# Kernel optimization log

Measured on AMD Instinct MI355X. Metric: run time of the kernel, lower is better.

Reference implementation:

```python
import jax, jax.numpy as jnp
import numpy as np

N = 12        # ALL_QUBITS
COM_Q = 9     # COM_QUBITS
IMG_Q = 11    # IMG_QUBITS
LAYERS = 2
SQRT2 = float(np.sqrt(2.0))
H_GATE = jnp.asarray([[1.0, 1.0], [1.0, -1.0]], dtype=jnp.complex64) / SQRT2


def _bitrev_perm(q):
    # column j of the wires-1..q subspace corresponds to param index bitrev(j)
    idx = np.arange(2 ** q)
    rev = np.zeros_like(idx)
    for bpos in range(q):
        rev |= ((idx >> bpos) & 1) << (q - 1 - bpos)
    return rev


def _apply_1q(state, U, w):
    # state: (B, 2^N) complex; apply 2x2 gate U on wire w (wire 0 = MSB)
    B = state.shape[0]
    s = state.reshape(B, 2 ** w, 2, -1)
    return jnp.einsum('ij,bpjq->bpiq', U, s).reshape(B, -1)


def _apply_cnot(state, c, t):
    B = state.shape[0]
    s = state.reshape((B,) + (2,) * N)
    s0 = jax.lax.slice_in_dim(s, 0, 1, axis=c + 1)
    s1 = jnp.flip(jax.lax.slice_in_dim(s, 1, 2, axis=c + 1), axis=t + 1)
    return jnp.concatenate([s0, s1], axis=c + 1).reshape(B, -1)


def _frqi(state, angles, q):
    # Hadamards on wires 1..q, then uniformly-controlled RY(angles) on wire 0
    for w in range(1, q + 1):
        state = _apply_1q(state, H_GATE, w)
    rev = _bitrev_perm(q)
    half = 0.5 * angles[:, rev]            # (B, 2^q), angle per control column
    c = jnp.cos(half)[:, :, None]
    s = jnp.sin(half)[:, :, None]
    B = state.shape[0]
    st = state.reshape(B, 2, 2 ** q, -1)   # (B, wire0, wires1..q, rest)
    new0 = c * st[:, 0] - s * st[:, 1]
    new1 = s * st[:, 0] + c * st[:, 1]
    return jnp.stack([new0, new1], axis=1).reshape(B, -1)


def _rot(phi, theta, omega):
    # PennyLane Rot = RZ(omega) RY(theta) RZ(phi)
    c = jnp.cos(theta / 2)
    s = jnp.sin(theta / 2)
    m00 = jnp.exp(-0.5j * (phi + omega)) * c
    m01 = -jnp.exp(0.5j * (phi - omega)) * s
    m10 = jnp.exp(-0.5j * (phi - omega)) * s
    m11 = jnp.exp(0.5j * (phi + omega)) * c
    return jnp.stack([jnp.stack([m00, m01]), jnp.stack([m10, m11])])


def _circuit(com_params, img_params, qp):
    B = com_params.shape[0]
    state = jnp.zeros((B, 2 ** N), jnp.complex64).at[:, 0].set(1.0)
    state = _frqi(state, com_params, COM_Q)
    for l in range(LAYERS):  # StronglyEntanglingLayers
        for w in range(N):
            state = _apply_1q(state, _rot(qp[l, w, 0], qp[l, w, 1], qp[l, w, 2]), w)
        r = l % (N - 1) + 1  # default ranges
        for w in range(N):
            state = _apply_cnot(state, w, (w + r) % N)
    state = _frqi(state, img_params, IMG_Q)
    p = (jnp.abs(state.reshape(B, 2, -1)) ** 2).sum(axis=2)  # (B, 2) wire-0 probs
    return p[:, 1] - p[:, 0]  # expval of Hamiltonian = -1 * Z(0)


def setup_inputs() -> dict:
    key = jax.random.key(0)
    k1, k2, k3 = jax.random.split(key, 3)
    B = 1024
    x = jax.random.uniform(k1, (B, 2, 32, 32), dtype=jnp.float32)
    W = jax.random.normal(k2, (512, 2048), dtype=jnp.float32) * 0.02
    b = jnp.zeros((512,), dtype=jnp.float32)
    quantum_params = jax.random.uniform(k3, (LAYERS, N, 3), dtype=jnp.float32) * float(np.pi)
    return {"x": x, "W": W, "b": b, "quantum_params": quantum_params}


def reference(x, W, b, quantum_params):
    B = x.shape[0]
    xf = x.reshape(B, -1)                 # (B, 2048) img_params
    com = xf @ W.T + b                    # (B, 512) classical_nn output
    return _circuit(com, xf, quantum_params)
```

## Files before the change

kernel.cpp:

```cpp
#include <hip/hip_runtime.h>
#include <hip/hip_bf16.h>
#include <math.h>

#define RS2f 0.70710678118654752f

typedef __attribute__((ext_vector_type(8))) short bf16x8;
typedef __attribute__((ext_vector_type(4))) float f32x4;

__device__ __forceinline__ float bf2f(unsigned short h) {
    return __uint_as_float(((unsigned)h) << 16);
}
__device__ __forceinline__ ushort2 pk2(float a, float b) {
    union { __hip_bfloat162 h; ushort2 s; } u;
    u.h = __float22bfloat162_rn(make_float2(a, b));
    return u.s;
}

struct CMat { float m00r,m00i,m01r,m01i,m10r,m10i,m11r,m11i; };

__device__ __forceinline__ CMat mk_rot(const float* __restrict__ qp, int l, int w) {
    const float* g = qp + (l * 12 + w) * 3;
    float phi = g[0], th = g[1], om = g[2];
    float st, ct, sa, ca, sb, cb;
    sincosf(0.5f * th, &st, &ct);
    sincosf(0.5f * (phi + om), &sa, &ca);
    sincosf(0.5f * (phi - om), &sb, &cb);
    CMat M;
    M.m00r =  ct * ca; M.m00i = -ct * sa;
    M.m01r = -st * cb; M.m01i = -st * sb;
    M.m10r =  st * cb; M.m10i = -st * sb;
    M.m11r =  ct * ca; M.m11i =  ct * sa;
    return M;
}

__global__ __launch_bounds__(512) void gemm_fused(const float* __restrict__ A,
                                                  const float* __restrict__ B,
                                                  float* __restrict__ P,
                                                  const float* __restrict__ qp,
                                                  CMat* __restrict__ cmg) {
    __shared__ short As[128 * 136];
    __shared__ short Bs[128 * 136];
    const int tid = threadIdx.x, lane = tid & 63, wv = tid >> 6;
    const int quad = lane >> 4, mrow = lane & 15;
    const int bid = blockIdx.x;
    if (bid == 0 && tid < 24) cmg[tid] = mk_rot(qp, tid / 12, tid % 12);
    const int zt  = bid & 7;
    const int idx = bid >> 3;
    const int mt  = idx & 7, nt = idx >> 3;
    const int m0 = mt * 128, n0 = nt * 128;
    const int kb = zt * 256;
    const int srow = tid >> 2;
    const int sc = (tid & 3) * 16;

    f32x4 acc[8];
    #pragma unroll
    for (int j = 0; j < 8; ++j) acc[j] = (f32x4){0.f, 0.f, 0.f, 0.f};

    const float* Arow = A + (size_t)(m0 + srow) * 2048 + kb + sc;
    const float* Brow = B + (size_t)(n0 + srow) * 2048 + kb + sc;

    float4 av[4], bv[4];
    #pragma unroll
    for (int i = 0; i < 4; ++i) { av[i] = *(const float4*)(Arow + 4*i);
                                  bv[i] = *(const float4*)(Brow + 4*i); }

    for (int ch = 0; ch < 4; ++ch) {
        __syncthreads();
        #pragma unroll
        for (int i = 0; i < 4; ++i) {
            ushort2 h0 = pk2(av[i].x, av[i].y);
            ushort2 h1 = pk2(av[i].z, av[i].w);
            ushort2 l0 = pk2(av[i].x - bf2f(h0.x), av[i].y - bf2f(h0.y));
            ushort2 l1 = pk2(av[i].z - bf2f(h1.x), av[i].w - bf2f(h1.y));
            *(ushort4*)&As[srow * 136 + sc + 4*i]      = make_ushort4(h0.x, h0.y, h1.x, h1.y);
            *(ushort4*)&As[srow * 136 + 64 + sc + 4*i] = make_ushort4(l0.x, l0.y, l1.x, l1.y);
            h0 = pk2(bv[i].x, bv[i].y);
            h1 = pk2(bv[i].z, bv[i].w);
            l0 = pk2(bv[i].x - bf2f(h0.x), bv[i].y - bf2f(h0.y));
            l1 = pk2(bv[i].z - bf2f(h1.x), bv[i].w - bf2f(h1.y));
            *(ushort4*)&Bs[srow * 136 + sc + 4*i]      = make_ushort4(h0.x, h0.y, h1.x, h1.y);
            *(ushort4*)&Bs[srow * 136 + 64 + sc + 4*i] = make_ushort4(l0.x, l0.y, l1.x, l1.y);
        }
        __syncthreads();
        if (ch + 1 < 4) {
            const int o = (ch + 1) * 64;
            #pragma unroll
            for (int i = 0; i < 4; ++i) { av[i] = *(const float4*)(Arow + o + 4*i);
                                          bv[i] = *(const float4*)(Brow + o + 4*i); }
        }
        #pragma unroll
        for (int s = 0; s < 4; ++s) {
            const int off = s * 32 + quad * 8;
            bf16x8 af = *(const bf16x8*)&As[(wv * 16 + mrow) * 136 + off];
            #pragma unroll
            for (int j = 0; j < 8; ++j) {
                bf16x8 bf = *(const bf16x8*)&Bs[(j * 16 + mrow) * 136 + off];
                acc[j] = __builtin_amdgcn_mfma_f32_16x16x32_bf16(af, bf, acc[j], 0, 0, 0);
            }
        }
    }
    float* Pz = P + (size_t)zt * 524288;
    #pragma unroll
    for (int j = 0; j < 8; ++j)
        #pragma unroll
        for (int r = 0; r < 4; ++r)
            Pz[(m0 + wv * 16 + quad * 4 + r) * 512 + n0 + j * 16 + mrow] = acc[j][r];
}

__global__ __launch_bounds__(256) void gemm_f32(const float* __restrict__ A,
                                                const float* __restrict__ W,
                                                float* __restrict__ C,
                                                const float* __restrict__ qp,
                                                CMat* __restrict__ cmg) {
    __shared__ float Asf[64][33];
    __shared__ float Bsf[32][33];
    const int tid = threadIdx.x;
    if (blockIdx.x == 0 && blockIdx.y == 0 && tid < 24)
        cmg[tid] = mk_rot(qp, tid / 12, tid % 12);
    const int m0 = blockIdx.x * 64;
    const int n0 = blockIdx.y * 32;
    const int tm = tid >> 4, tn = tid & 15;
    float acc[4][2] = {};
    for (int k0 = 0; k0 < 2048; k0 += 32) {
        #pragma unroll
        for (int i = 0; i < 8; ++i) {
            int idx = tid + i * 256;
            Asf[idx >> 5][idx & 31] = A[(m0 + (idx >> 5)) * 2048 + k0 + (idx & 31)];
        }
        #pragma unroll
        for (int i = 0; i < 4; ++i) {
            int idx = tid + i * 256;
            Bsf[idx >> 5][idx & 31] = W[(n0 + (idx >> 5)) * 2048 + k0 + (idx & 31)];
        }
        __syncthreads();
        #pragma unroll
        for (int kk = 0; kk < 32; ++kk) {
            float a0 = Asf[tm*4+0][kk], a1 = Asf[tm*4+1][kk];
            float a2 = Asf[tm*4+2][kk], a3 = Asf[tm*4+3][kk];
            float b0 = Bsf[tn*2+0][kk], b1 = Bsf[tn*2+1][kk];
            acc[0][0] += a0*b0; acc[0][1] += a0*b1;
            acc[1][0] += a1*b0; acc[1][1] += a1*b1;
            acc[2][0] += a2*b0; acc[2][1] += a2*b1;
            acc[3][0] += a3*b0; acc[3][1] += a3*b1;
        }
        __syncthreads();
    }
    #pragma unroll
    for (int r = 0; r < 4; ++r)
        #pragma unroll
        for (int c = 0; c < 2; ++c)
            C[(m0 + tm*4 + r) * 512 + n0 + tn*2 + c] = acc[r][c];
}

template<int W> struct WI {
    static constexpr int kind = (W == 0 || W == 7) ? 2 : ((W >= 1 && W <= 6) ? 1 : 0);
    static constexpr int eb   = (W >= 8) ? (11 - W) : 0;
    static constexpr int lm   = (W >= 1 && W <= 6) ? (1 << (6 - W)) : 0;
    static constexpr int vm   = (W == 0) ? 2 : ((W == 7) ? 1 : 0);
};

__device__ __forceinline__ void exch_put(float* xbuf, int slot,
                                         const float vr[16], const float vi[16]) {
    __syncthreads();
    float4* p = (float4*)xbuf;
    #pragma unroll
    for (int j = 0; j < 8; ++j)
        p[(j << 8) + slot] = make_float4(vr[2*j], vi[2*j], vr[2*j+1], vi[2*j+1]);
    __syncthreads();
}

__device__ __forceinline__ void shfl_perm(float vr[16], float vi[16], int src) {
    #pragma unroll
    for (int e = 0; e < 16; ++e) {
        vr[e] = __shfl(vr[e], src, 64);
        vi[e] = __shfl(vi[e], src, 64);
    }
}

template<int EB>
__device__ __forceinline__ void rot_local(float vr[16], float vi[16], const CMat& M) {
    #pragma unroll
    for (int e = 0; e < 16; ++e) if (!(e & (1 << EB))) {
        const int e1 = e | (1 << EB);
        float x0r = vr[e],  x0i = vi[e];
        float x1r = vr[e1], x1i = vi[e1];
        vr[e]  = M.m00r*x0r - M.m00i*x0i + M.m01r*x1r - M.m01i*x1i;
        vi[e]  = M.m00r*x0i + M.m00i*x0r + M.m01r*x1i + M.m01i*x1r;
        vr[e1] = M.m10r*x0r - M.m10i*x0i + M.m11r*x1r - M.m11i*x1i;
        vi[e1] = M.m10r*x0i + M.m10i*x0r + M.m11r*x1i + M.m11i*x1r;
    }
}

template<int LM>
__device__ __forceinline__ void rot_lane(float vr[16], float vi[16], int lane, const CMat& M) {
    const bool hi = lane & LM;
    const float Ar = hi ? M.m11r : M.m00r, Ai = hi ? M.m11i : M.m00i;
    const float Br = hi ? M.m10r : M.m01r, Bi = hi ? M.m10i : M.m01i;
    #pragma unroll
    for (int e = 0; e < 16; ++e) {
        float pr = __shfl_xor(vr[e], LM, 64);
        float pi = __shfl_xor(vi[e], LM, 64);
        float orr = vr[e], oi = vi[e];
        vr[e] = Ar*orr - Ai*oi + Br*pr - Bi*pi;
        vi[e] = Ar*oi + Ai*orr + Br*pi + Bi*pr;
    }
}

template<int VM>
__device__ __forceinline__ void rot_wave(float vr[16], float vi[16], float* xbuf,
                                         int waveId, int lane, const CMat& M) {
    exch_put(xbuf, (waveId << 6) + lane, vr, vi);
    const float4* p = (const float4*)xbuf;
    const int ps = ((waveId ^ VM) << 6) + lane;
    const bool hi = waveId & VM;
    const float Ar = hi ? M.m11r : M.m00r, Ai = hi ? M.m11i : M.m00i;
    const float Br = hi ? M.m10r : M.m01r, Bi = hi ? M.m10i : M.m01i;
    #pragma unroll
    for (int j = 0; j < 8; ++j) {
        float4 q = p[(j << 8) + ps];
        const int e0 = 2*j, e1 = 2*j + 1;
        float r0 = vr[e0], i0 = vi[e0], r1 = vr[e1], i1 = vi[e1];
        vr[e0] = Ar*r0 - Ai*i0 + Br*q.x - Bi*q.y;
        vi[e0] = Ar*i0 + Ai*r0 + Br*q.y + Bi*q.x;
        vr[e1] = Ar*r1 - Ai*i1 + Br*q.z - Bi*q.w;
        vi[e1] = Ar*i1 + Ai*r1 + Br*q.w + Bi*q.z;
    }
}

template<int W>
__device__ __forceinline__ void rot_wire(float vr[16], float vi[16], float* xbuf,
                                         int waveId, int lane, const CMat& M) {
    if constexpr (WI<W>::kind == 0)      rot_local<WI<W>::eb>(vr, vi, M);
    else if constexpr (WI<W>::kind == 1) rot_lane<WI<W>::lm>(vr, vi, lane, M);
    else                                 rot_wave<WI<W>::vm>(vr, vi, xbuf, waveId, lane, M);
}

template<int C, int T>
__device__ __forceinline__ void cnot(float vr[16], float vi[16], float* xbuf,
                                     int waveId, int lane) {
    constexpr int ck = WI<C>::kind, tk = WI<T>::kind;
    if constexpr (ck == 0 && tk == 0) {
        constexpr int cb = 1 << WI<C>::eb, tb = 1 << WI<T>::eb;
        #pragma unroll
        for (int e = 0; e < 16; ++e) if ((e & cb) && !(e & tb)) {
            const int e1 = e | tb;
            float t = vr[e]; vr[e] = vr[e1]; vr[e1] = t;
            t = vi[e]; vi[e] = vi[e1]; vi[e1] = t;
        }
    } else if constexpr (ck == 0 && tk == 1) {
        constexpr int cb = 1 << WI<C>::eb, tm = WI<T>::lm;
        #pragma unroll
        for (int e = 0; e < 16; ++e) if (e & cb) {
            vr[e] = __shfl_xor(vr[e], tm, 64);
            vi[e] = __shfl_xor(vi[e], tm, 64);
        }
    } else if constexpr (ck == 0 && tk == 2) {
        constexpr int cb = 1 << WI<C>::eb, vm = WI<T>::vm;
        exch_put(xbuf, (waveId << 6) + lane, vr, vi);
        const float4* p = (const float4*)xbuf;
        const int ps = ((waveId ^ vm) << 6) + lane;
        #pragma unroll
        for (int j = 0; j < 8; ++j) {
            if ((((2*j) & cb) != 0) || (((2*j+1) & cb) != 0)) {
                float4 q = p[(j << 8) + ps];
                if (((2*j) & cb) != 0)   { vr[2*j]   = q.x; vi[2*j]   = q.y; }
                if (((2*j+1) & cb) != 0) { vr[2*j+1] = q.z; vi[2*j+1] = q.w; }
            }
        }
    } else if constexpr (ck == 1 && tk == 0) {
        constexpr int cm = WI<C>::lm, tb = 1 << WI<T>::eb;
        const bool cc = lane & cm;
        #pragma unroll
        for (int e = 0; e < 16; ++e) if (!(e & tb)) {
            const int e1 = e | tb;
            float a = vr[e], bb = vr[e1];
            vr[e] = cc ? bb : a; vr[e1] = cc ? a : bb;
            a = vi[e]; bb = vi[e1];
            vi[e] = cc ? bb : a; vi[e1] = cc ? a : bb;
        }
    } else if constexpr (ck == 1 && tk == 1) {
        constexpr int cm = WI<C>::lm, tm = WI<T>::lm;
        const int src = (lane & cm) ? (lane ^ tm) : lane;
        shfl_perm(vr, vi, src);
    } else if constexpr (ck == 1 && tk == 2) {
        constexpr int cm = WI<C>::lm, vm = WI<T>::vm;
        exch_put(xbuf, (waveId << 6) + lane, vr, vi);
        const float4* p = (const float4*)xbuf;
        const int ps = ((waveId ^ vm) << 6) + lane;
        const bool take = lane & cm;
        #pragma unroll
        for (int j = 0; j < 8; ++j) {
            float4 q = p[(j << 8) + ps];
            vr[2*j]   = take ? q.x : vr[2*j];   vi[2*j]   = take ? q.y : vi[2*j];
            vr[2*j+1] = take ? q.z : vr[2*j+1]; vi[2*j+1] = take ? q.w : vi[2*j+1];
        }
    } else if constexpr (ck == 2 && tk == 0) {
        constexpr int vm = WI<C>::vm, tb = 1 << WI<T>::eb;
        if (waveId & vm) {
            #pragma unroll
            for (int e = 0; e < 16; ++e) if (!(e & tb)) {
                const int e1 = e | tb;
                float t = vr[e]; vr[e] = vr[e1]; vr[e1] = t;
                t = vi[e]; vi[e] = vi[e1]; vi[e1] = t;
            }
        }
    } else {
        constexpr int vm = WI<C>::vm, tm = WI<T>::lm;
        if (waveId & vm) {
            #pragma unroll
            for (int e = 0; e < 16; ++e) {
                vr[e] = __shfl_xor(vr[e], tm, 64);
                vi[e] = __shfl_xor(vi[e], tm, 64);
            }
        }
    }
}

template<int W>
__device__ __forceinline__ void h_wire(float vr[16], float vi[16], float* xbuf,
                                       int waveId, int lane) {
    if constexpr (WI<W>::kind == 0) {
        constexpr int tb = 1 << WI<W>::eb;
        #pragma unroll
        for (int e = 0; e < 16; ++e) if (!(e & tb)) {
            const int e1 = e | tb;
            float x0 = vr[e], x1 = vr[e1];
            vr[e] = (x0 + x1) * RS2f; vr[e1] = (x0 - x1) * RS2f;
            x0 = vi[e]; x1 = vi[e1];
            vi[e] = (x0 + x1) * RS2f; vi[e1] = (x0 - x1) * RS2f;
        }
    } else if constexpr (WI<W>::kind == 1) {
        constexpr int m = WI<W>::lm;
        const float sgn = (lane & m) ? -RS2f : RS2f;
        #pragma unroll
        for (int e = 0; e < 16; ++e) {
            float pr = __shfl_xor(vr[e], m, 64);
            float pi = __shfl_xor(vi[e], m, 64);
            vr[e] = pr * RS2f + vr[e] * sgn;
            vi[e] = pi * RS2f + vi[e] * sgn;
        }
    } else {
        constexpr int vm = WI<W>::vm;
        exch_put(xbuf, (waveId << 6) + lane, vr, vi);
        const float4* p = (const float4*)xbuf;
        const int ps = ((waveId ^ vm) << 6) + lane;
        const float sgn = (waveId & vm) ? -RS2f : RS2f;
        #pragma unroll
        for (int j = 0; j < 8; ++j) {
            float4 q = p[(j << 8) + ps];
            vr[2*j]   = q.x * RS2f + vr[2*j]   * sgn;
            vi[2*j]   = q.y * RS2f + vi[2*j]   * sgn;
            vr[2*j+1] = q.z * RS2f + vr[2*j+1] * sgn;
            vi[2*j+1] = q.w * RS2f + vi[2*j+1] * sgn;
        }
    }
}

__global__ __launch_bounds__(256) void circuit_red(const float* __restrict__ P,
                                                   const float* __restrict__ xf,
                                                   const CMat* __restrict__ cmg,
                                                   const float* __restrict__ bias,
                                                   float* __restrict__ out, int SK) {
    __shared__ float xbuf[8192];
    const int tid = threadIdx.x, lane = tid & 63, waveId = tid >> 6;
    const int b = blockIdx.x;
    {
        float2 s = ((const float2*)bias)[tid];
        for (int z = 0; z < SK; ++z) {
            float2 q = ((const float2*)(P + (size_t)z * 524288 + (size_t)b * 512))[tid];
            s.x += q.x; s.y += q.y;
        }
        ((float2*)xbuf)[tid] = s;
    }
    __syncthreads();
    float vr[16], vi[16];
    #pragma unroll
    for (int e = 0; e < 16; ++e) { vr[e] = 0.0f; vi[e] = 0.0f; }
    const float K9 = 0.044194173824159216f;
    #pragma unroll
    for (int m = 0; m < 4; ++m) {
        int j = (lane << 3) | ((waveId & 1) << 2) | m;
        int rj = (int)(__brev((unsigned)j) >> 23);
        float h = 0.5f * xbuf[rj];
        float s = __sinf(h), c = __cosf(h);
        vr[m << 2] = K9 * ((waveId & 2) ? s : c);
    }
    #pragma unroll 1
    for (int l = 0; l < 2; ++l) {
        const CMat* cl = cmg + l * 12;
        { CMat M = cl[0];  rot_wire<0 >(vr, vi, xbuf, waveId, lane, M); }
        { CMat M = cl[1];  rot_wire<1 >(vr, vi, xbuf, waveId, lane, M); }
        { CMat M = cl[2];  rot_wire<2 >(vr, vi, xbuf, waveId, lane, M); }
        { CMat M = cl[3];  rot_wire<3 >(vr, vi, xbuf, waveId, lane, M); }
        { CMat M = cl[4];  rot_wire<4 >(vr, vi, xbuf, waveId, lane, M); }
        { CMat M = cl[5];  rot_wire<5 >(vr, vi, xbuf, waveId, lane, M); }
        { CMat M = cl[6];  rot_wire<6 >(vr, vi, xbuf, waveId, lane, M); }
        { CMat M = cl[7];  rot_wire<7 >(vr, vi, xbuf, waveId, lane, M); }
        { CMat M = cl[8];  rot_wire<8 >(vr, vi, xbuf, waveId, lane, M); }
        { CMat M = cl[9];  rot_wire<9 >(vr, vi, xbuf, waveId, lane, M); }
        { CMat M = cl[10]; rot_wire<10>(vr, vi, xbuf, waveId, lane, M); }
        { CMat M = cl[11]; rot_wire<11>(vr, vi, xbuf, waveId, lane, M); }
        if (l == 0) {
            int j = lane;
            j ^= (j & 2)  ? 1  : 0;
            j ^= (j & 4)  ? 2  : 0;
            j ^= (j & 8)  ? 4  : 0;
            j ^= (j & 16) ? 8  : 0;
            j ^= (j & 32) ? 16 : 0;
            j ^= (waveId & 2) ? 32 : 0;
            shfl_perm(vr, vi, j);
            cnot<6,7>(vr,vi,xbuf,waveId,lane);   cnot<7,8>(vr,vi,xbuf,waveId,lane);
            cnot<8,9>(vr,vi,xbuf,waveId,lane);   cnot<9,10>(vr,vi,xbuf,waveId,lane);
            cnot<10,11>(vr,vi,xbuf,waveId,lane); cnot<11,0>(vr,vi,xbuf,waveId,lane);
        } else {
            int j = lane;
            j ^= (j & 4)  ? 1  : 0;
            j ^= (j & 8)  ? 2  : 0;
            j ^= (j & 16) ? 4  : 0;
            j ^= (j & 32) ? 8  : 0;
            j ^= (waveId & 2) ? 16 : 0;
            shfl_perm(vr, vi, j);
            cnot<5,7>(vr,vi,xbuf,waveId,lane);   cnot<6,8>(vr,vi,xbuf,waveId,lane);
            cnot<7,9>(vr,vi,xbuf,waveId,lane);   cnot<8,10>(vr,vi,xbuf,waveId,lane);
            cnot<9,11>(vr,vi,xbuf,waveId,lane);  cnot<10,0>(vr,vi,xbuf,waveId,lane);
            cnot<11,1>(vr,vi,xbuf,waveId,lane);
        }
    }
    h_wire<1>(vr,vi,xbuf,waveId,lane);  h_wire<2>(vr,vi,xbuf,waveId,lane);
    h_wire<3>(vr,vi,xbuf,waveId,lane);  h_wire<4>(vr,vi,xbuf,waveId,lane);
    h_wire<5>(vr,vi,xbuf,waveId,lane);  h_wire<6>(vr,vi,xbuf,waveId,lane);
    h_wire<7>(vr,vi,xbuf,waveId,lane);  h_wire<8>(vr,vi,xbuf,waveId,lane);
    h_wire<9>(vr,vi,xbuf,waveId,lane);  h_wire<10>(vr,vi,xbuf,waveId,lane);
    h_wire<11>(vr,vi,xbuf,waveId,lane);
    exch_put(xbuf, (waveId << 6) + lane, vr, vi);
    {
        const float* xrow = xf + (size_t)b * 2048;
        const float4* p = (const float4*)xbuf;
        const int ps = ((waveId ^ 2) << 6) + lane;
        const bool hi = waveId & 2;
        float acc = 0.0f;
        #pragma unroll
        for (int j = 0; j < 8; ++j) {
            float4 q = p[(j << 8) + ps];
            #pragma unroll
            for (int h = 0; h < 2; ++h) {
                const int e = 2*j + h;
                const float prr = h ? q.z : q.x;
                const float pii = h ? q.w : q.y;
                int v = (lane << 5) | ((waveId & 1) << 4) | e;
                int rv = (int)(__brev((unsigned)v) >> 21);
                float ha = 0.5f * xrow[rv];
                float s = __sinf(ha), c = __cosf(ha);
                float nr = hi ? (s*prr + c*vr[e]) : (c*vr[e] - s*prr);
                float ni = hi ? (s*pii + c*vi[e]) : (c*vi[e] - s*pii);
                acc += nr*nr + ni*ni;
            }
        }
        if (!hi) acc = -acc;
        #pragma unroll
        for (int off = 32; off > 0; off >>= 1) acc += __shfl_down(acc, off, 64);
        __syncthreads();
        if (lane == 0) xbuf[waveId] = acc;
        __syncthreads();
        if (tid == 0) out[b] = xbuf[0] + xbuf[1] + xbuf[2] + xbuf[3];
    }
}

extern "C" void kernel_launch(void* const* d_in, const int* in_sizes, int n_in,
                              void* d_out, int out_size, void* d_ws, size_t ws_size,
                              hipStream_t stream) {
    const float* x    = (const float*)d_in[0];
    const float* W    = (const float*)d_in[1];
    const float* bias = (const float*)d_in[2];
    const float* qp   = (const float*)d_in[3];
    float* out = (float*)d_out;

    const size_t SLAB = 2097152;
    const size_t CMSZ = 1024;
    float* P = (float*)d_ws;

    if (ws_size >= 8 * SLAB + CMSZ) {
        CMat* cmg = (CMat*)((char*)d_ws + 8 * SLAB);
        gemm_fused<<<256, 512, 0, stream>>>(x, W, P, qp, cmg);
        circuit_red<<<1024, 256, 0, stream>>>(P, x, cmg, bias, out, 8);
    } else {
        CMat* cmg = (CMat*)((char*)d_ws + SLAB);
        dim3 g(16, 16);
        gemm_f32<<<g, 256, 0, stream>>>(x, W, P, qp, cmg);
        circuit_red<<<1024, 256, 0, stream>>>(P, x, cmg, bias, out, 1);
    }
}
```

Measured before the change: 139.9 us.

## Fuse split-K GEMM and circuit simulation into one cooperative kernel with grid sync

Replaces the two-kernel sequence (split-K bf16x3 GEMM, then per-sample circuit simulation) with one cooperative kernel of 1024 blocks. Each block first computes a 64x64 GEMM tile for one K-slice, using an XCD-aware tile mapping, then all blocks meet at a grid-wide barrier. After that each block runs the circuit body for one batch row, reusing the same shared-memory buffer. This is meant to remove the gap between kernel launches and the tail of the first kernel. In exchange it needs all 1024 blocks resident at once (4 per CU), which caps registers for the circuit code and adds the cost of a grid sync. If the cooperative launch fails, it falls back to the old two kernels.

```diff
diff --git a/kernel.cpp b/kernel.cpp
--- a/kernel.cpp
+++ b/kernel.cpp
@@ -1,6 +1,9 @@
 #include <hip/hip_runtime.h>
+#include <hip/hip_cooperative_groups.h>
 #include <hip/hip_bf16.h>
 #include <math.h>
+
+namespace cg = cooperative_groups;
 
 #define RS2f 0.70710678118654752f
 
@@ -33,125 +36,6 @@
     return M;
 }
 
-__global__ __launch_bounds__(512) void gemm_fused(const float* __restrict__ A,
-                                                  const float* __restrict__ B,
-                                                  float* __restrict__ P,
-                                                  const float* __restrict__ qp,
-                                                  CMat* __restrict__ cmg) {
-    __shared__ short As[128 * 136];
-    __shared__ short Bs[128 * 136];
-    const int tid = threadIdx.x, lane = tid & 63, wv = tid >> 6;
-    const int quad = lane >> 4, mrow = lane & 15;
-    const int bid = blockIdx.x;
-    if (bid == 0 && tid < 24) cmg[tid] = mk_rot(qp, tid / 12, tid % 12);
-    const int zt  = bid & 7;
-    const int idx = bid >> 3;
-    const int mt  = idx & 7, nt = idx >> 3;
-    const int m0 = mt * 128, n0 = nt * 128;
-    const int kb = zt * 256;
-    const int srow = tid >> 2;
-    const int sc = (tid & 3) * 16;
-
-    f32x4 acc[8];
-    #pragma unroll
-    for (int j = 0; j < 8; ++j) acc[j] = (f32x4){0.f, 0.f, 0.f, 0.f};
-
-    const float* Arow = A + (size_t)(m0 + srow) * 2048 + kb + sc;
-    const float* Brow = B + (size_t)(n0 + srow) * 2048 + kb + sc;
-
-    float4 av[4], bv[4];
-    #pragma unroll
-    for (int i = 0; i < 4; ++i) { av[i] = *(const float4*)(Arow + 4*i);
-                                  bv[i] = *(const float4*)(Brow + 4*i); }
-
-    for (int ch = 0; ch < 4; ++ch) {
-        __syncthreads();
-        #pragma unroll
-        for (int i = 0; i < 4; ++i) {
-            ushort2 h0 = pk2(av[i].x, av[i].y);
-            ushort2 h1 = pk2(av[i].z, av[i].w);
-            ushort2 l0 = pk2(av[i].x - bf2f(h0.x), av[i].y - bf2f(h0.y));
-            ushort2 l1 = pk2(av[i].z - bf2f(h1.x), av[i].w - bf2f(h1.y));
-            *(ushort4*)&As[srow * 136 + sc + 4*i]      = make_ushort4(h0.x, h0.y, h1.x, h1.y);
-            *(ushort4*)&As[srow * 136 + 64 + sc + 4*i] = make_ushort4(l0.x, l0.y, l1.x, l1.y);
-            h0 = pk2(bv[i].x, bv[i].y);
-            h1 = pk2(bv[i].z, bv[i].w);
-            l0 = pk2(bv[i].x - bf2f(h0.x), bv[i].y - bf2f(h0.y));
-            l1 = pk2(bv[i].z - bf2f(h1.x), bv[i].w - bf2f(h1.y));
-            *(ushort4*)&Bs[srow * 136 + sc + 4*i]      = make_ushort4(h0.x, h0.y, h1.x, h1.y);
-            *(ushort4*)&Bs[srow * 136 + 64 + sc + 4*i] = make_ushort4(l0.x, l0.y, l1.x, l1.y);
-        }
-        __syncthreads();
-        if (ch + 1 < 4) {
-            const int o = (ch + 1) * 64;
-            #pragma unroll
-            for (int i = 0; i < 4; ++i) { av[i] = *(const float4*)(Arow + o + 4*i);
-                                          bv[i] = *(const float4*)(Brow + o + 4*i); }
-        }
-        #pragma unroll
-        for (int s = 0; s < 4; ++s) {
-            const int off = s * 32 + quad * 8;
-            bf16x8 af = *(const bf16x8*)&As[(wv * 16 + mrow) * 136 + off];
-            #pragma unroll
-            for (int j = 0; j < 8; ++j) {
-                bf16x8 bf = *(const bf16x8*)&Bs[(j * 16 + mrow) * 136 + off];
-                acc[j] = __builtin_amdgcn_mfma_f32_16x16x32_bf16(af, bf, acc[j], 0, 0, 0);
-            }
-        }
-    }
-    float* Pz = P + (size_t)zt * 524288;
-    #pragma unroll
-    for (int j = 0; j < 8; ++j)
-        #pragma unroll
-        for (int r = 0; r < 4; ++r)
-            Pz[(m0 + wv * 16 + quad * 4 + r) * 512 + n0 + j * 16 + mrow] = acc[j][r];
-}
-
-__global__ __launch_bounds__(256) void gemm_f32(const float* __restrict__ A,
-                                                const float* __restrict__ W,
-                                                float* __restrict__ C,
-                                                const float* __restrict__ qp,
-                                                CMat* __restrict__ cmg) {
-    __shared__ float Asf[64][33];
-    __shared__ float Bsf[32][33];
-    const int tid = threadIdx.x;
-    if (blockIdx.x == 0 && blockIdx.y == 0 && tid < 24)
-        cmg[tid] = mk_rot(qp, tid / 12, tid % 12);
-    const int m0 = blockIdx.x * 64;
-    const int n0 = blockIdx.y * 32;
-    const int tm = tid >> 4, tn = tid & 15;
-    float acc[4][2] = {};
-    for (int k0 = 0; k0 < 2048; k0 += 32) {
-        #pragma unroll
-        for (int i = 0; i < 8; ++i) {
-            int idx = tid + i * 256;
-            Asf[idx >> 5][idx & 31] = A[(m0 + (idx >> 5)) * 2048 + k0 + (idx & 31)];
-        }
-        #pragma unroll
-        for (int i = 0; i < 4; ++i) {
-            int idx = tid + i * 256;
-            Bsf[idx >> 5][idx & 31] = W[(n0 + (idx >> 5)) * 2048 + k0 + (idx & 31)];
-        }
-        __syncthreads();
-        #pragma unroll
-        for (int kk = 0; kk < 32; ++kk) {
-            float a0 = Asf[tm*4+0][kk], a1 = Asf[tm*4+1][kk];
-            float a2 = Asf[tm*4+2][kk], a3 = Asf[tm*4+3][kk];
-            float b0 = Bsf[tn*2+0][kk], b1 = Bsf[tn*2+1][kk];
-            acc[0][0] += a0*b0; acc[0][1] += a0*b1;
-            acc[1][0] += a1*b0; acc[1][1] += a1*b1;
-            acc[2][0] += a2*b0; acc[2][1] += a2*b1;
-            acc[3][0] += a3*b0; acc[3][1] += a3*b1;
-        }
-        __syncthreads();
-    }
-    #pragma unroll
-    for (int r = 0; r < 4; ++r)
-        #pragma unroll
-        for (int c = 0; c < 2; ++c)
-            C[(m0 + tm*4 + r) * 512 + n0 + tn*2 + c] = acc[r][c];
-}
-
 template<int W> struct WI {
     static constexpr int kind = (W == 0 || W == 7) ? 2 : ((W >= 1 && W <= 6) ? 1 : 0);
     static constexpr int eb   = (W >= 8) ? (11 - W) : 0;
@@ -356,14 +240,13 @@
     }
 }
 
-__global__ __launch_bounds__(256) void circuit_red(const float* __restrict__ P,
-                                                   const float* __restrict__ xf,
-                                                   const CMat* __restrict__ cmg,
-                                                   const float* __restrict__ bias,
-                                                   float* __restrict__ out, int SK) {
-    __shared__ float xbuf[8192];
+__device__ __forceinline__ void circuit_body(float* xbuf, int b,
+                                             const float* __restrict__ P,
+                                             const float* __restrict__ xf,
+                                             const CMat* __restrict__ cmg,
+                                             const float* __restrict__ bias,
+                                             float* __restrict__ out, int SK) {
     const int tid = threadIdx.x, lane = tid & 63, waveId = tid >> 6;
-    const int b = blockIdx.x;
     {
         float2 s = ((const float2*)bias)[tid];
         for (int z = 0; z < SK; ++z) {
@@ -466,6 +349,220 @@
     }
 }
 
+__global__ __launch_bounds__(256, 4) void fused_all(const float* __restrict__ A,
+                                                    const float* __restrict__ B,
+                                                    const float* __restrict__ bias,
+                                                    const float* __restrict__ qp,
+                                                    float* __restrict__ P,
+                                                    CMat* __restrict__ cmg,
+                                                    float* __restrict__ out) {
+    __shared__ __align__(16) char lds[34816];
+    short* As   = (short*)lds;
+    short* Bs   = (short*)(lds + 17408);
+    float* xbuf = (float*)lds;
+    const int tid = threadIdx.x, lane = tid & 63, wv = tid >> 6;
+    const int quad = lane >> 4, mrow = lane & 15;
+    const int bid = blockIdx.x;
+
+    if (bid == 0 && tid < 24) cmg[tid] = mk_rot(qp, tid / 12, tid % 12);
+    {
+        const int xcd = bid & 7;
+        const int idx = bid >> 3;
+        const int mt  = ((xcd >> 1) << 2) | (idx & 3);
+        const int nt  = ((xcd & 1) << 2) | ((idx >> 2) & 3);
+        const int zt  = idx >> 4;
+        const int m0 = mt * 64, n0 = nt * 64;
+        const int kb = zt * 256;
+        const int srow = tid >> 2;
+        const int sc = (tid & 3) * 16;
+
+        f32x4 acc[4];
+        #pragma unroll
+        for (int j = 0; j < 4; ++j) acc[j] = (f32x4){0.f, 0.f, 0.f, 0.f};
+
+        const float* Arow = A + (size_t)(m0 + srow) * 2048 + kb + sc;
+        const float* Brow = B + (size_t)(n0 + srow) * 2048 + kb + sc;
+
+        float4 av[4], bv[4];
+        #pragma unroll
+        for (int i = 0; i < 4; ++i) { av[i] = *(const float4*)(Arow + 4*i);
+                                      bv[i] = *(const float4*)(Brow + 4*i); }
+
+        for (int ch = 0; ch < 4; ++ch) {
+            __syncthreads();
+            #pragma unroll
+            for (int i = 0; i < 4; ++i) {
+                ushort2 h0 = pk2(av[i].x, av[i].y);
+                ushort2 h1 = pk2(av[i].z, av[i].w);
+                ushort2 l0 = pk2(av[i].x - bf2f(h0.x), av[i].y - bf2f(h0.y));
+                ushort2 l1 = pk2(av[i].z - bf2f(h1.x), av[i].w - bf2f(h1.y));
+                *(ushort4*)&As[srow * 136 + sc + 4*i]      = make_ushort4(h0.x, h0.y, h1.x, h1.y);
+                *(ushort4*)&As[srow * 136 + 64 + sc + 4*i] = make_ushort4(l0.x, l0.y, l1.x, l1.y);
+                h0 = pk2(bv[i].x, bv[i].y);
+                h1 = pk2(bv[i].z, bv[i].w);
+                l0 = pk2(bv[i].x - bf2f(h0.x), bv[i].y - bf2f(h0.y));
+                l1 = pk2(bv[i].z - bf2f(h1.x), bv[i].w - bf2f(h1.y));
+                *(ushort4*)&Bs[srow * 136 + sc + 4*i]      = make_ushort4(h0.x, h0.y, h1.x, h1.y);
+                *(ushort4*)&Bs[srow * 136 + 64 + sc + 4*i] = make_ushort4(l0.x, l0.y, l1.x, l1.y);
+            }
+            __syncthreads();
+            if (ch + 1 < 4) {
+                const int o = (ch + 1) * 64;
+                #pragma unroll
+                for (int i = 0; i < 4; ++i) { av[i] = *(const float4*)(Arow + o + 4*i);
+                                              bv[i] = *(const float4*)(Brow + o + 4*i); }
+            }
+            #pragma unroll
+            for (int s = 0; s < 4; ++s) {
+                const int off = s * 32 + quad * 8;
+                bf16x8 af = *(const bf16x8*)&As[(wv * 16 + mrow) * 136 + off];
+                #pragma unroll
+                for (int j = 0; j < 4; ++j) {
+                    bf16x8 bf = *(const bf16x8*)&Bs[(j * 16 + mrow) * 136 + off];
+                    acc[j] = __builtin_amdgcn_mfma_f32_16x16x32_bf16(af, bf, acc[j], 0, 0, 0);
+                }
+            }
+        }
+        float* Pz = P + (size_t)zt * 524288;
+        #pragma unroll
+        for (int j = 0; j < 4; ++j)
+            #pragma unroll
+            for (int r = 0; r < 4; ++r)
+                Pz[(m0 + wv * 16 + quad * 4 + r) * 512 + n0 + j * 16 + mrow] = acc[j][r];
+    }
+    __threadfence();
+    cg::this_grid().sync();
+    circuit_body(xbuf, bid, P, A, cmg, bias, out, 8);
+}
+
+__global__ __launch_bounds__(512) void gemm_fused(const float* __restrict__ A,
+                                                  const float* __restrict__ B,
+                                                  float* __restrict__ P,
+                                                  const float* __restrict__ qp,
+                                                  CMat* __restrict__ cmg) {
+    __shared__ short As[128 * 136];
+    __shared__ short Bs[128 * 136];
+    const int tid = threadIdx.x, lane = tid & 63, wv = tid >> 6;
+    const int quad = lane >> 4, mrow = lane & 15;
+    const int bid = blockIdx.x;
+    if (bid == 0 && tid < 24) cmg[tid] = mk_rot(qp, tid / 12, tid % 12);
+    const int zt  = bid & 7;
+    const int idx = bid >> 3;
+    const int mt  = idx & 7, nt = idx >> 3;
+    const int m0 = mt * 128, n0 = nt * 128;
+    const int kb = zt * 256;
+    const int srow = tid >> 2;
+    const int sc = (tid & 3) * 16;
+
+    f32x4 acc[8];
+    #pragma unroll
+    for (int j = 0; j < 8; ++j) acc[j] = (f32x4){0.f, 0.f, 0.f, 0.f};
+
+    const float* Arow = A + (size_t)(m0 + srow) * 2048 + kb + sc;
+    const float* Brow = B + (size_t)(n0 + srow) * 2048 + kb + sc;
+
+    float4 av[4], bv[4];
+    #pragma unroll
+    for (int i = 0; i < 4; ++i) { av[i] = *(const float4*)(Arow + 4*i);
+                                  bv[i] = *(const float4*)(Brow + 4*i); }
+
+    for (int ch = 0; ch < 4; ++ch) {
+        __syncthreads();
+        #pragma unroll
+        for (int i = 0; i < 4; ++i) {
+            ushort2 h0 = pk2(av[i].x, av[i].y);
+            ushort2 h1 = pk2(av[i].z, av[i].w);
+            ushort2 l0 = pk2(av[i].x - bf2f(h0.x), av[i].y - bf2f(h0.y));
+            ushort2 l1 = pk2(av[i].z - bf2f(h1.x), av[i].w - bf2f(h1.y));
+            *(ushort4*)&As[srow * 136 + sc + 4*i]      = make_ushort4(h0.x, h0.y, h1.x, h1.y);
+            *(ushort4*)&As[srow * 136 + 64 + sc + 4*i] = make_ushort4(l0.x, l0.y, l1.x, l1.y);
+            h0 = pk2(bv[i].x, bv[i].y);
+            h1 = pk2(bv[i].z, bv[i].w);
+            l0 = pk2(bv[i].x - bf2f(h0.x), bv[i].y - bf2f(h0.y));
+            l1 = pk2(bv[i].z - bf2f(h1.x), bv[i].w - bf2f(h1.y));
+            *(ushort4*)&Bs[srow * 136 + sc + 4*i]      = make_ushort4(h0.x, h0.y, h1.x, h1.y);
+            *(ushort4*)&Bs[srow * 136 + 64 + sc + 4*i] = make_ushort4(l0.x, l0.y, l1.x, l1.y);
+        }
+        __syncthreads();
+        if (ch + 1 < 4) {
+            const int o = (ch + 1) * 64;
+            #pragma unroll
+            for (int i = 0; i < 4; ++i) { av[i] = *(const float4*)(Arow + o + 4*i);
+                                          bv[i] = *(const float4*)(Brow + o + 4*i); }
+        }
+        #pragma unroll
+        for (int s = 0; s < 4; ++s) {
+            const int off = s * 32 + quad * 8;
+            bf16x8 af = *(const bf16x8*)&As[(wv * 16 + mrow) * 136 + off];
+            #pragma unroll
+            for (int j = 0; j < 8; ++j) {
+                bf16x8 bf = *(const bf16x8*)&Bs[(j * 16 + mrow) * 136 + off];
+                acc[j] = __builtin_amdgcn_mfma_f32_16x16x32_bf16(af, bf, acc[j], 0, 0, 0);
+            }
+        }
+    }
+    float* Pz = P + (size_t)zt * 524288;
+    #pragma unroll
+    for (int j = 0; j < 8; ++j)
+        #pragma unroll
+        for (int r = 0; r < 4; ++r)
+            Pz[(m0 + wv * 16 + quad * 4 + r) * 512 + n0 + j * 16 + mrow] = acc[j][r];
+}
+
+__global__ __launch_bounds__(256) void circuit_red(const float* __restrict__ P,
+                                                   const float* __restrict__ xf,
+                                                   const CMat* __restrict__ cmg,
+                                                   const float* __restrict__ bias,
+                                                   float* __restrict__ out, int SK) {
+    __shared__ float xbuf[8192];
+    circuit_body(xbuf, blockIdx.x, P, xf, cmg, bias, out, SK);
+}
+
+__global__ __launch_bounds__(256) void gemm_f32(const float* __restrict__ A,
+                                                const float* __restrict__ W,
+                                                float* __restrict__ C,
+                                                const float* __restrict__ qp,
+                                                CMat* __restrict__ cmg) {
+    __shared__ float Asf[64][33];
+    __shared__ float Bsf[32][33];
+    const int tid = threadIdx.x;
+    if (blockIdx.x == 0 && blockIdx.y == 0 && tid < 24)
+        cmg[tid] = mk_rot(qp, tid / 12, tid % 12);
+    const int m0 = blockIdx.x * 64;
+    const int n0 = blockIdx.y * 32;
+    const int tm = tid >> 4, tn = tid & 15;
+    float acc[4][2] = {};
+    for (int k0 = 0; k0 < 2048; k0 += 32) {
+        #pragma unroll
+        for (int i = 0; i < 8; ++i) {
+            int idx = tid + i * 256;
+            Asf[idx >> 5][idx & 31] = A[(m0 + (idx >> 5)) * 2048 + k0 + (idx & 31)];
+        }
+        #pragma unroll
+        for (int i = 0; i < 4; ++i) {
+            int idx = tid + i * 256;
+            Bsf[idx >> 5][idx & 31] = W[(n0 + (idx >> 5)) * 2048 + k0 + (idx & 31)];
+        }
+        __syncthreads();
+        #pragma unroll
+        for (int kk = 0; kk < 32; ++kk) {
+            float a0 = Asf[tm*4+0][kk], a1 = Asf[tm*4+1][kk];
+            float a2 = Asf[tm*4+2][kk], a3 = Asf[tm*4+3][kk];
+            float b0 = Bsf[tn*2+0][kk], b1 = Bsf[tn*2+1][kk];
+            acc[0][0] += a0*b0; acc[0][1] += a0*b1;
+            acc[1][0] += a1*b0; acc[1][1] += a1*b1;
+            acc[2][0] += a2*b0; acc[2][1] += a2*b1;
+            acc[3][0] += a3*b0; acc[3][1] += a3*b1;
+        }
+        __syncthreads();
+    }
+    #pragma unroll
+    for (int r = 0; r < 4; ++r)
+        #pragma unroll
+        for (int c = 0; c < 2; ++c)
+            C[(m0 + tm*4 + r) * 512 + n0 + tn*2 + c] = acc[r][c];
+}
+
 extern "C" void kernel_launch(void* const* d_in, const int* in_sizes, int n_in,
                               void* d_out, int out_size, void* d_ws, size_t ws_size,
                               hipStream_t stream) {
@@ -481,8 +578,16 @@
 
     if (ws_size >= 8 * SLAB + CMSZ) {
         CMat* cmg = (CMat*)((char*)d_ws + 8 * SLAB);
-        gemm_fused<<<256, 512, 0, stream>>>(x, W, P, qp, cmg);
-        circuit_red<<<1024, 256, 0, stream>>>(P, x, cmg, bias, out, 8);
+        void* args[] = { (void*)&x, (void*)&W, (void*)&bias, (void*)&qp,
+                         (void*)&P, (void*)&cmg, (void*)&out };
+        hipError_t e = hipLaunchCooperativeKernel((const void*)fused_all,
+                                                  dim3(1024), dim3(256),
+                                                  args, 0, stream);
+        if (e != hipSuccess) {
+            (void)hipGetLastError();
+            gemm_fused<<<256, 512, 0, stream>>>(x, W, P, qp, cmg);
+            circuit_red<<<1024, 256, 0, stream>>>(P, x, cmg, bias, out, 8);
+        }
     } else {
         CMat* cmg = (CMat*)((char*)d_ws + SLAB);
         dim3 g(16, 16);
```

Result: slower. 355.2 us (+153.9%).
